# Kernel optimization log

Measured on AMD Instinct MI355X. Metric: run time of the kernel, lower is better.

The kernel has to match this reference:

```python
import jax, jax.numpy as jnp
import numpy as np

TAU = 2.0
BN_EPS = 1e-5
SG_ALPHA = 4.0
ATTN_SCALE = 0.125
NUM_HEADS = 8
T, B, C, H, W = 2, 16, 256, 64, 64


@jax.custom_vjp
def heaviside(x):
    return (x >= 0.0).astype(x.dtype)

def _hv_fwd(x):
    return (x >= 0.0).astype(x.dtype), x

def _hv_bwd(x, g):
    s = jax.nn.sigmoid(SG_ALPHA * x)
    return (g * SG_ALPHA * s * (1.0 - s),)

heaviside.defvjp(_hv_fwd, _hv_bwd)


def lif(x_seq, v_th):
    # MultiStepLIFNode: v <- v + (x - v)/tau ; spike = H(v - v_th); hard reset to 0 (detached)
    def step(v, x):
        v = v + (x - v) / TAU
        s = heaviside(v - v_th)
        v = v * (1.0 - jax.lax.stop_gradient(s))
        return v, s
    _, spikes = jax.lax.scan(step, jnp.zeros_like(x_seq[0]), x_seq)
    return spikes


def bn1d(x, gamma, beta, mean, var):
    # eval-mode BatchNorm1d over channel axis 2 of [T,B,C,N]
    inv = (gamma / jnp.sqrt(var + BN_EPS)).reshape(1, 1, -1, 1)
    shift = (beta - mean * gamma / jnp.sqrt(var + BN_EPS)).reshape(1, 1, -1, 1)
    return x * inv + shift


def to_heads(t):
    # [T,B,C,N] -> [T,B,h,N,d]
    t_, b_, c_, n_ = t.shape
    d = c_ // NUM_HEADS
    return t.transpose(0, 1, 3, 2).reshape(t_, b_, n_, NUM_HEADS, d).transpose(0, 1, 3, 2, 4)


def setup_inputs() -> dict:
    key = jax.random.key(0)
    ks = jax.random.split(key, 24)
    w_scale = 0.06  # ~1/sqrt(C)
    inp = {
        'x': jax.random.normal(ks[0], (T, B, C, H, W), jnp.float32),
        'wq': jax.random.normal(ks[1], (C, C), jnp.float32) * w_scale,
        'wk': jax.random.normal(ks[2], (C, C), jnp.float32) * w_scale,
        'wv': jax.random.normal(ks[3], (C, C), jnp.float32) * w_scale,
        'wp': jax.random.normal(ks[4], (C, C), jnp.float32) * w_scale,
        'bp': jax.random.normal(ks[5], (C,), jnp.float32) * 0.1,
    }
    i = 6
    for p in ('q', 'k', 'v', 'p'):
        inp[p + '_gamma'] = jax.random.uniform(ks[i], (C,), jnp.float32, 0.5, 1.5); i += 1
        inp[p + '_beta'] = jax.random.normal(ks[i], (C,), jnp.float32) * 0.1; i += 1
        inp[p + '_mean'] = jax.random.normal(ks[i], (C,), jnp.float32) * 0.1; i += 1
        inp[p + '_var'] = jax.random.uniform(ks[i], (C,), jnp.float32, 0.5, 1.5); i += 1
    return inp


def reference(x, wq, wk, wv, wp, bp,
              q_gamma, q_beta, q_mean, q_var,
              k_gamma, k_beta, k_mean, k_var,
              v_gamma, v_beta, v_mean, v_var,
              p_gamma, p_beta, p_mean, p_var):
    t_, b_, c_, h_, w_ = x.shape
    n_ = h_ * w_
    xs = lif(x, 1.0).reshape(t_, b_, c_, n_)  # proj_lif then flatten(3)
    # 1x1 conv == channel matmul, then BN, then LIF (binary spikes)
    q_out = lif(bn1d(jnp.einsum('oc,tbcn->tbon', wq, xs), q_gamma, q_beta, q_mean, q_var), 1.0)
    k_out = lif(bn1d(jnp.einsum('oc,tbcn->tbon', wk, xs), k_gamma, k_beta, k_mean, k_var), 1.0)
    v_out = lif(bn1d(jnp.einsum('oc,tbcn->tbon', wv, xs), v_gamma, v_beta, v_mean, v_var), 1.0)
    q = to_heads(q_out)
    k = to_heads(k_out)
    v = to_heads(v_out)
    # linear attention: (k^T @ v) then q @ (k^T v)
    kv = jnp.einsum('tbhnd,tbhne->tbhde', k, v)  # [T,B,h,d,d]
    attn = jnp.einsum('tbhnd,tbhde->tbhne', q, kv) * ATTN_SCALE
    attn = attn.transpose(0, 1, 2, 4, 3).reshape(t_, b_, c_, n_)
    s = lif(attn, 0.5)  # attn_lif with v_threshold=0.5
    out = jnp.einsum('oc,tbcn->tbon', wp, s) + bp.reshape(1, 1, -1, 1)
    out = bn1d(out, p_gamma, p_beta, p_mean, p_var).reshape(t_, b_, c_, h_, w_)
    return (out, xs, q_out, k_out, v_out)
```

## Files before the change

kernel.cpp:

```cpp
#include <hip/hip_runtime.h>
#include <cstdint>
#include <cstddef>

typedef __attribute__((ext_vector_type(8))) short short8;
typedef __attribute__((ext_vector_type(4))) float floatx4;
typedef __attribute__((ext_vector_type(4))) unsigned int uintx4;
typedef __attribute__((ext_vector_type(4))) unsigned short ushort4x;

#define DEV static __device__ __forceinline__

constexpr int NT = 2, NB = 16, NC = 256, NN = 4096, NHD = 8;
constexpr size_t NE1 = (size_t)NT * NB * NC * NN;
constexpr size_t TSTRIDE = (size_t)NB * NC * NN;

DEV unsigned short f2bf(float x) {
  unsigned int u = __builtin_bit_cast(unsigned int, x);
  unsigned int lsb = (u >> 16) & 1u;
  u += 0x7FFFu + lsb;
  return (unsigned short)(u >> 16);
}
DEV float bfb2f(unsigned short h) {
  unsigned int u = ((unsigned int)h) << 16;
  return __builtin_bit_cast(float, u);
}
DEV unsigned short spike2bf(float s) {
  return (unsigned short)(__builtin_bit_cast(unsigned int, s) >> 16);
}
DEV unsigned int pk2(unsigned short a, unsigned short b) {
  return (unsigned int)a | ((unsigned int)b << 16);
}
typedef __attribute__((address_space(3))) unsigned int lds_u32;
typedef __attribute__((address_space(1))) const unsigned int glb_u32;
DEV void gld_lds16(const void* g, void* l) {
  __builtin_amdgcn_global_load_lds((glb_u32*)g, (lds_u32*)l, 16, 0, 0);
}

__global__ __launch_bounds__(256) void prep_kernel(
    const float* __restrict__ wq, const float* __restrict__ wk, const float* __restrict__ wv,
    const float* __restrict__ wp, const float* __restrict__ bp,
    const float* __restrict__ qg, const float* __restrict__ qb, const float* __restrict__ qm, const float* __restrict__ qva,
    const float* __restrict__ kg, const float* __restrict__ kb, const float* __restrict__ km, const float* __restrict__ kva,
    const float* __restrict__ vg, const float* __restrict__ vb, const float* __restrict__ vm, const float* __restrict__ vva,
    const float* __restrict__ pg, const float* __restrict__ pb, const float* __restrict__ pm, const float* __restrict__ pva,
    unsigned short* __restrict__ Wqkv, unsigned short* __restrict__ Wp,
    float* __restrict__ invqkv, float* __restrict__ shqkv,
    float* __restrict__ invp, float* __restrict__ shp)
{
  int idx = blockIdx.x * 256 + threadIdx.x;
  if (idx < 196608) {
    int o = idx >> 8, c = idx & 255;
    const float* src = (o < 256) ? wq : (o < 512) ? wk : wv;
    float w = src[(size_t)(o & 255) * 256 + c];
    unsigned short h0 = f2bf(w);  float f0 = bfb2f(h0);
    float r1 = w - f0;
    unsigned short h1 = f2bf(r1); float f1 = bfb2f(h1);
    float r2 = r1 - f1;
    unsigned short h2 = f2bf(r2);
    Wqkv[idx] = h0; Wqkv[196608 + idx] = h1; Wqkv[393216 + idx] = h2;
  } else if (idx < 262144) {
    int j = idx - 196608;
    float w = wp[j];
    unsigned short h0 = f2bf(w);  float f0 = bfb2f(h0);
    float r1 = w - f0;
    unsigned short h1 = f2bf(r1); float f1 = bfb2f(h1);
    float r2 = r1 - f1;
    unsigned short h2 = f2bf(r2);
    Wp[j] = h0; Wp[65536 + j] = h1; Wp[131072 + j] = h2;
  } else if (idx < 262912) {
    int i = idx - 262144;
    int p = i >> 8, c = i & 255;
    float g  = (p == 0) ? qg[c] : (p == 1) ? kg[c] : vg[c];
    float be = (p == 0) ? qb[c] : (p == 1) ? kb[c] : vb[c];
    float mn = (p == 0) ? qm[c] : (p == 1) ? km[c] : vm[c];
    float vr = (p == 0) ? qva[c] : (p == 1) ? kva[c] : vva[c];
    float sq = sqrtf(vr + 1e-5f);
    invqkv[i] = g / sq;
    shqkv[i]  = be - (mn * g) / sq;
  } else if (idx < 263168) {
    int c = idx - 262912;
    float sq = sqrtf(pva[c] + 1e-5f);
    float iv = pg[c] / sq;
    invp[c] = iv;
    shp[c]  = pb[c] - (pm[c] * pg[c]) / sq + bp[c] * iv;
  }
}

__global__ __launch_bounds__(256) void lifx_kernel(const float* __restrict__ x,
                                                   float* __restrict__ xs_out,
                                                   unsigned short* __restrict__ xs_t)
{
  __shared__ float tile[2][64][65];
  const int nt = blockIdx.x, ct = blockIdx.y, b = blockIdx.z;
  const int tid = threadIdx.x;
  const int ci = tid >> 2, cq = tid & 3;
  const int n0 = nt * 64, c0 = ct * 64;
  const size_t rowbase = ((size_t)(b * NC + c0 + ci)) * NN + n0 + cq * 16;
  const float* px0 = x + rowbase;
  const float* px1 = x + rowbase + TSTRIDE;
  float* po0 = xs_out + rowbase;
  float* po1 = xs_out + rowbase + TSTRIDE;
  #pragma unroll
  for (int jj = 0; jj < 4; jj++) {
    floatx4 x0 = *(const floatx4*)(px0 + jj * 4);
    floatx4 x1 = *(const floatx4*)(px1 + jj * 4);
    floatx4 s0v, s1v;
    #pragma unroll
    for (int e = 0; e < 4; e++) {
      float v1 = x0[e] * 0.5f;
      float s0 = (v1 >= 1.0f) ? 1.0f : 0.0f;
      float vr = v1 * (1.0f - s0);
      float v2 = vr + (x1[e] - vr) * 0.5f;
      float s1 = (v2 >= 1.0f) ? 1.0f : 0.0f;
      s0v[e] = s0; s1v[e] = s1;
      tile[0][ci][cq * 16 + jj * 4 + e] = s0;
      tile[1][ci][cq * 16 + jj * 4 + e] = s1;
    }
    *(floatx4*)(po0 + jj * 4) = s0v;
    *(floatx4*)(po1 + jj * 4) = s1v;
  }
  __syncthreads();
  const int ni = tid >> 2, cg = tid & 3;
  #pragma unroll
  for (int t = 0; t < 2; t++) {
    unsigned short* dst = xs_t + ((size_t)((t * NB + b) * NN) + n0 + ni) * NC + c0 + cg * 16;
    uintx4 w0, w1;
    #pragma unroll
    for (int p2 = 0; p2 < 4; p2++) {
      w0[p2] = pk2(spike2bf(tile[t][cg * 16 + p2 * 2    ][ni]),
                   spike2bf(tile[t][cg * 16 + p2 * 2 + 1][ni]));
      w1[p2] = pk2(spike2bf(tile[t][cg * 16 + p2 * 2 + 8][ni]),
                   spike2bf(tile[t][cg * 16 + p2 * 2 + 9][ni]));
    }
    *(uintx4*)dst = w0;
    *(uintx4*)(dst + 8) = w1;
  }
}

__global__ __launch_bounds__(256, 3) void qkv_gemm(
    const unsigned short* __restrict__ xs_t,
    const unsigned short* __restrict__ Wsp,
    const float* __restrict__ invv, const float* __restrict__ shv,
    float* __restrict__ dq, float* __restrict__ dk, float* __restrict__ dv)
{
  __shared__ __align__(16) unsigned char smem[33280];
  unsigned short* Al = (unsigned short*)smem;
  unsigned short* Bl = (unsigned short*)(smem + 24576);
  float* yl = (float*)smem;
  const int nt = blockIdx.x, mt = blockIdx.y, b = blockIdx.z;
  const int tid = threadIdx.x;
  const int lane = tid & 63, quad = lane >> 4, l16 = lane & 15;
  const int wave = tid >> 6;
  const int tw = wave >> 1, wm = (wave & 1) * 64;
  floatx4 acc[4][4] = {};

  for (int k0 = 0; k0 < 256; k0 += 32) {
    __syncthreads();
    #pragma unroll
    for (int j = 0; j < 6; j++) {
      int ci = j * 256 + tid;
      int s = ci >> 9, j2 = ci & 511, row = j2 >> 2, kk = j2 & 3;
      const unsigned short* g = Wsp + (size_t)s * 196608 + (size_t)(mt * 128 + row) * 256 + k0 + kk * 8;
      gld_lds16(g, Al + ci * 8);
    }
    #pragma unroll
    for (int j = 0; j < 2; j++) {
      int ci = j * 256 + tid;
      int t = ci >> 8, j2 = ci & 255, row = j2 >> 2, kk = j2 & 3;
      const unsigned short* g = xs_t + ((size_t)((t * NB + b) * NN) + nt * 64 + row) * NC + k0 + kk * 8;
      gld_lds16(g, Bl + ci * 8);
    }
    __syncthreads();

    short8 bfr[4];
    #pragma unroll
    for (int ni = 0; ni < 4; ni++)
      bfr[ni] = *(const short8*)(Bl + ((size_t)(tw * 64 + ni * 16 + l16)) * 32 + quad * 8);
    #pragma unroll
    for (int mi = 0; mi < 4; mi++) {
      const int arow = wm + mi * 16 + l16;
      short8 a0 = *(const short8*)(Al + ((size_t)(          arow)) * 32 + quad * 8);
      short8 a1 = *(const short8*)(Al + ((size_t)(128  +   arow)) * 32 + quad * 8);
      short8 a2 = *(const short8*)(Al + ((size_t)(256  +   arow)) * 32 + quad * 8);
      #pragma unroll
      for (int ni = 0; ni < 4; ni++) {
        acc[mi][ni] = __builtin_amdgcn_mfma_f32_16x16x32_bf16(a0, bfr[ni], acc[mi][ni], 0, 0, 0);
        acc[mi][ni] = __builtin_amdgcn_mfma_f32_16x16x32_bf16(a1, bfr[ni], acc[mi][ni], 0, 0, 0);
        acc[mi][ni] = __builtin_amdgcn_mfma_f32_16x16x32_bf16(a2, bfr[ni], acc[mi][ni], 0, 0, 0);
      }
    }
  }
  __syncthreads();
  if (tw == 0) {
    #pragma unroll
    for (int mi = 0; mi < 4; mi++)
      #pragma unroll
      for (int r = 0; r < 4; r++)
        #pragma unroll
        for (int ni = 0; ni < 4; ni++)
          yl[(size_t)(wm + mi * 16 + quad * 4 + r) * 65 + ni * 16 + l16] = acc[mi][ni][r];
  }
  __syncthreads();
  if (tw == 1) {
    #pragma unroll
    for (int mi = 0; mi < 4; mi++) {
      #pragma unroll
      for (int r = 0; r < 4; r++) {
        const int lrow = wm + mi * 16 + quad * 4 + r;
        const int orow = mt * 128 + lrow;
        const float iv = invv[orow], sh = shv[orow];
        const int widx = orow >> 8, c = orow & 255;
        float* dst = (widx == 0) ? dq : (widx == 1) ? dk : dv;
        #pragma unroll
        for (int ni = 0; ni < 4; ni++) {
          const int n = nt * 64 + ni * 16 + l16;
          float y0 = yl[(size_t)lrow * 65 + ni * 16 + l16] * iv + sh;
          float y1 = acc[mi][ni][r] * iv + sh;
          float v1 = y0 * 0.5f;
          float s0 = (v1 >= 1.0f) ? 1.0f : 0.0f;
          float vr = v1 * (1.0f - s0);
          float v2 = vr + (y1 - vr) * 0.5f;
          float s1 = (v2 >= 1.0f) ? 1.0f : 0.0f;
          dst[(size_t)(b * NC + c) * NN + n] = s0;
          dst[(size_t)((NB + b) * NC + c) * NN + n] = s1;
        }
      }
    }
  }
}

__global__ __launch_bounds__(256) void kv_kernel(const float* __restrict__ kspk,
                                                 const float* __restrict__ vspk,
                                                 float* __restrict__ kvp)
{
  __shared__ __align__(16) unsigned short Kl[32][264];
  __shared__ __align__(16) unsigned short Vl[32][264];
  const int h = blockIdx.x, z = blockIdx.y, ch = blockIdx.z;
  const int tid = threadIdx.x;
  const int wave = tid >> 6, lane = tid & 63, quad = lane >> 4, l16 = lane & 15;
  const int dh = wave & 1, eh = wave >> 1;
  const size_t base = (size_t)z * NC * NN + (size_t)h * 32 * NN + (size_t)ch * 1024;
  floatx4 acc = {0.f, 0.f, 0.f, 0.f};
  for (int n0 = 0; n0 < 1024; n0 += 256) {
    __syncthreads();
    for (int i = tid; i < 2048; i += 256) {
      int row = i >> 6, c4 = (i & 63) * 4;
      const size_t g = base + (size_t)row * NN + n0 + c4;
      floatx4 kk = *(const floatx4*)(kspk + g);
      floatx4 vv = *(const floatx4*)(vspk + g);
      ushort4x ks, vs;
      #pragma unroll
      for (int e = 0; e < 4; e++) { ks[e] = spike2bf(kk[e]); vs[e] = spike2bf(vv[e]); }
      *(ushort4x*)&Kl[row][c4] = ks;
      *(ushort4x*)&Vl[row][c4] = vs;
    }
    __syncthreads();
    #pragma unroll
    for (int i = 0; i < 8; i++) {
      short8 ka = *(const short8*)&Kl[dh * 16 + l16][i * 32 + quad * 8];
      short8 vb = *(const short8*)&Vl[eh * 16 + l16][i * 32 + quad * 8];
      acc = __builtin_amdgcn_mfma_f32_16x16x32_bf16(ka, vb, acc, 0, 0, 0);
    }
  }
  float* o = kvp + ((size_t)((ch * 32 + z) * NHD + h)) * 1024;
  #pragma unroll
  for (int r = 0; r < 4; r++)
    o[(dh * 16 + quad * 4 + r) * 32 + eh * 16 + l16] = acc[r];
}

__global__ __launch_bounds__(256) void attn_kernel(const float* __restrict__ qspk,
                                                   const float* __restrict__ kvp,
                                                   unsigned short* __restrict__ s_t)
{
  __shared__ float kvl[2][32][32];
  const int nb = blockIdx.x, h = blockIdx.y, b = blockIdx.z;
  const int tid = threadIdx.x;
  for (int i = tid; i < 2048; i += 256) {
    int t = i >> 10, j = i & 1023;
    size_t o = ((size_t)((t * NB + b) * NHD + h) << 10) + j;
    float v = kvp[o] + kvp[o + 262144] + kvp[o + 524288] + kvp[o + 786432];
    kvl[t][j >> 5][j & 31] = v;
  }
  __syncthreads();
  const int n = nb * 256 + tid;
  float X[2][32];
  #pragma unroll
  for (int t = 0; t < 2; t++) {
    #pragma unroll
    for (int e = 0; e < 32; e++) X[t][e] = 0.f;
    const float* qp = qspk + ((size_t)((t * NB + b) * NC + h * 32)) * NN + n;
    #pragma unroll 4
    for (int d = 0; d < 32; d++) {
      float qv = qp[(size_t)d * NN];
      #pragma unroll
      for (int e = 0; e < 32; e++) X[t][e] += qv * kvl[t][d][e];
    }
  }
  unsigned short o0[32], o1[32];
  #pragma unroll
  for (int e = 0; e < 32; e++) {
    float a0 = X[0][e] * 0.125f;
    float a1 = X[1][e] * 0.125f;
    float v1 = a0 * 0.5f;
    float s0 = (v1 >= 0.5f) ? 1.f : 0.f;
    float vr = v1 * (1.f - s0);
    float v2 = vr + (a1 - vr) * 0.5f;
    float s1 = (v2 >= 0.5f) ? 1.f : 0.f;
    o0[e] = s0 != 0.f ? (unsigned short)0x3F80 : (unsigned short)0;
    o1[e] = s1 != 0.f ? (unsigned short)0x3F80 : (unsigned short)0;
  }
  unsigned short* dst0 = s_t + ((size_t)(b * NN) + n) * NC + h * 32;
  unsigned short* dst1 = s_t + ((size_t)((NB + b) * NN) + n) * NC + h * 32;
  #pragma unroll
  for (int g = 0; g < 4; g++) {
    uintx4 w0, w1;
    #pragma unroll
    for (int p = 0; p < 4; p++) {
      w0[p] = pk2(o0[g * 8 + p * 2], o0[g * 8 + p * 2 + 1]);
      w1[p] = pk2(o1[g * 8 + p * 2], o1[g * 8 + p * 2 + 1]);
    }
    *(uintx4*)(dst0 + g * 8) = w0;
    *(uintx4*)(dst1 + g * 8) = w1;
  }
}

__global__ __launch_bounds__(256, 3) void p_gemm(
    const unsigned short* __restrict__ s_t,
    const unsigned short* __restrict__ Wsp,
    const float* __restrict__ invv, const float* __restrict__ shv,
    float* __restrict__ dout)
{
  __shared__ __align__(16) unsigned char smem[32768];
  unsigned short* Al = (unsigned short*)smem;
  unsigned short* Bl = (unsigned short*)(smem + 24576);
  const int nt = blockIdx.x, mt = blockIdx.y, z = blockIdx.z;
  const int tid = threadIdx.x;
  const int lane = tid & 63, quad = lane >> 4, l16 = lane & 15;
  const int wave = tid >> 6;
  const int wm = (wave & 1) * 64, wn = (wave >> 1) * 64;
  floatx4 acc[4][4] = {};

  for (int k0 = 0; k0 < 256; k0 += 32) {
    __syncthreads();
    #pragma unroll
    for (int j = 0; j < 6; j++) {
      int ci = j * 256 + tid;
      int s = ci >> 9, j2 = ci & 511, row = j2 >> 2, kk = j2 & 3;
      const unsigned short* g = Wsp + (size_t)s * 65536 + (size_t)(mt * 128 + row) * 256 + k0 + kk * 8;
      gld_lds16(g, Al + ci * 8);
    }
    #pragma unroll
    for (int j = 0; j < 2; j++) {
      int ci = j * 256 + tid;
      int row = ci >> 2, kk = ci & 3;
      const unsigned short* g = s_t + ((size_t)(z * NN) + nt * 128 + row) * NC + k0 + kk * 8;
      gld_lds16(g, Bl + ci * 8);
    }
    __syncthreads();

    short8 bfr[4];
    #pragma unroll
    for (int ni = 0; ni < 4; ni++)
      bfr[ni] = *(const short8*)(Bl + ((size_t)(wn + ni * 16 + l16)) * 32 + quad * 8);
    #pragma unroll
    for (int mi = 0; mi < 4; mi++) {
      const int arow = wm + mi * 16 + l16;
      short8 a0 = *(const short8*)(Al + ((size_t)(        arow)) * 32 + quad * 8);
      short8 a1 = *(const short8*)(Al + ((size_t)(128 +   arow)) * 32 + quad * 8);
      short8 a2 = *(const short8*)(Al + ((size_t)(256 +   arow)) * 32 + quad * 8);
      #pragma unroll
      for (int ni = 0; ni < 4; ni++) {
        acc[mi][ni] = __builtin_amdgcn_mfma_f32_16x16x32_bf16(a0, bfr[ni], acc[mi][ni], 0, 0, 0);
        acc[mi][ni] = __builtin_amdgcn_mfma_f32_16x16x32_bf16(a1, bfr[ni], acc[mi][ni], 0, 0, 0);
        acc[mi][ni] = __builtin_amdgcn_mfma_f32_16x16x32_bf16(a2, bfr[ni], acc[mi][ni], 0, 0, 0);
      }
    }
  }
  #pragma unroll
  for (int mi = 0; mi < 4; mi++) {
    #pragma unroll
    for (int r = 0; r < 4; r++) {
      const int orow = mt * 128 + wm + mi * 16 + quad * 4 + r;
      const float iv = invv[orow], sh = shv[orow];
      #pragma unroll
      for (int ni = 0; ni < 4; ni++) {
        const int n = nt * 128 + wn + ni * 16 + l16;
        dout[((size_t)(z * NC + orow)) * NN + n] = acc[mi][ni][r] * iv + sh;
      }
    }
  }
}

extern "C" void kernel_launch(void* const* d_in, const int* in_sizes, int n_in,
                              void* d_out, int out_size, void* d_ws, size_t ws_size,
                              hipStream_t stream) {
  (void)in_sizes; (void)n_in; (void)out_size; (void)ws_size;
  const float* x  = (const float*)d_in[0];
  const float* wq = (const float*)d_in[1];
  const float* wk = (const float*)d_in[2];
  const float* wv = (const float*)d_in[3];
  const float* wp = (const float*)d_in[4];
  const float* bp = (const float*)d_in[5];
  const float* qg = (const float*)d_in[6],  *qb = (const float*)d_in[7];
  const float* qm = (const float*)d_in[8],  *qva = (const float*)d_in[9];
  const float* kg = (const float*)d_in[10], *kb = (const float*)d_in[11];
  const float* km = (const float*)d_in[12], *kva = (const float*)d_in[13];
  const float* vg = (const float*)d_in[14], *vb = (const float*)d_in[15];
  const float* vm = (const float*)d_in[16], *vva = (const float*)d_in[17];
  const float* pg = (const float*)d_in[18], *pb = (const float*)d_in[19];
  const float* pm = (const float*)d_in[20], *pva = (const float*)d_in[21];

  float* out = (float*)d_out;
  float* xs  = out + NE1;
  float* dq  = out + 2 * NE1;
  float* dk  = out + 3 * NE1;
  float* dv  = out + 4 * NE1;

  char* ws = (char*)d_ws;
  unsigned short* xs_t = (unsigned short*)ws;
  unsigned short* s_t  = (unsigned short*)ws;
  unsigned short* Wqkv = (unsigned short*)(ws + 67108864);
  unsigned short* Wp   = (unsigned short*)(ws + 68288512);
  float* kvp           = (float*)(ws + 68681728);
  float* invqkv        = (float*)(ws + 72876032);
  float* shqkv         = invqkv + 768;
  float* invp          = shqkv + 768;
  float* shp           = invp + 256;

  prep_kernel<<<1028, 256, 0, stream>>>(wq, wk, wv, wp, bp,
                                        qg, qb, qm, qva, kg, kb, km, kva,
                                        vg, vb, vm, vva, pg, pb, pm, pva,
                                        Wqkv, Wp, invqkv, shqkv, invp, shp);
  lifx_kernel<<<dim3(64, 4, 16), 256, 0, stream>>>(x, xs, xs_t);
  qkv_gemm<<<dim3(64, 6, 16), 256, 0, stream>>>(xs_t, Wqkv, invqkv, shqkv, dq, dk, dv);
  kv_kernel<<<dim3(8, 32, 4), 256, 0, stream>>>(dk, dv, kvp);
  attn_kernel<<<dim3(16, 8, 16), 256, 0, stream>>>(dq, kvp, s_t);
  p_gemm<<<dim3(32, 2, 32), 256, 0, stream>>>(s_t, Wp, invp, shp, out);
}
```

Measured before the change: 1.128 ms.

## Compute q·kv in attention kernel with bf16 MFMA using split-precision kv

Replaces the per-thread scalar FMA loop over 32x32 kv in attn_kernel with MFMA 16x16x32 bf16 instructions. The q spike tile is staged in padded LDS, and kv is split into high and low bf16 parts so that two MFMAs approximate fp32 precision. The aim is to remove the heavy FMA and LDS-broadcast cost. In exchange it writes output spikes as scattered 2-byte stores instead of 16-byte vectors, and the two-term bf16 split can still flip spikes that sit right at the threshold.

```diff
diff --git a/kernel.cpp b/kernel.cpp
--- a/kernel.cpp
+++ b/kernel.cpp
@@ -271,9 +271,11 @@
                                                    const float* __restrict__ kvp,
                                                    unsigned short* __restrict__ s_t)
 {
-  __shared__ float kvl[2][32][32];
+  __shared__ float kvl[2][32][33];
+  __shared__ __align__(8) float ql[32][258];
   const int nb = blockIdx.x, h = blockIdx.y, b = blockIdx.z;
   const int tid = threadIdx.x;
+  const int wave = tid >> 6, lane = tid & 63, quad = lane >> 4, l16 = lane & 15;
   for (int i = tid; i < 2048; i += 256) {
     int t = i >> 10, j = i & 1023;
     size_t o = ((size_t)((t * NB + b) * NHD + h) << 10) + j;
@@ -281,45 +283,68 @@
     kvl[t][j >> 5][j & 31] = v;
   }
   __syncthreads();
-  const int n = nb * 256 + tid;
-  float X[2][32];
+  short8 bf[2][2][2];
   #pragma unroll
   for (int t = 0; t < 2; t++) {
     #pragma unroll
-    for (int e = 0; e < 32; e++) X[t][e] = 0.f;
-    const float* qp = qspk + ((size_t)((t * NB + b) * NC + h * 32)) * NN + n;
-    #pragma unroll 4
-    for (int d = 0; d < 32; d++) {
-      float qv = qp[(size_t)d * NN];
-      #pragma unroll
-      for (int e = 0; e < 32; e++) X[t][e] += qv * kvl[t][d][e];
-    }
-  }
-  unsigned short o0[32], o1[32];
-  #pragma unroll
-  for (int e = 0; e < 32; e++) {
-    float a0 = X[0][e] * 0.125f;
-    float a1 = X[1][e] * 0.125f;
-    float v1 = a0 * 0.5f;
-    float s0 = (v1 >= 0.5f) ? 1.f : 0.f;
-    float vr = v1 * (1.f - s0);
-    float v2 = vr + (a1 - vr) * 0.5f;
-    float s1 = (v2 >= 0.5f) ? 1.f : 0.f;
-    o0[e] = s0 != 0.f ? (unsigned short)0x3F80 : (unsigned short)0;
-    o1[e] = s1 != 0.f ? (unsigned short)0x3F80 : (unsigned short)0;
-  }
-  unsigned short* dst0 = s_t + ((size_t)(b * NN) + n) * NC + h * 32;
-  unsigned short* dst1 = s_t + ((size_t)((NB + b) * NN) + n) * NC + h * 32;
-  #pragma unroll
-  for (int g = 0; g < 4; g++) {
-    uintx4 w0, w1;
-    #pragma unroll
-    for (int p = 0; p < 4; p++) {
-      w0[p] = pk2(o0[g * 8 + p * 2], o0[g * 8 + p * 2 + 1]);
-      w1[p] = pk2(o1[g * 8 + p * 2], o1[g * 8 + p * 2 + 1]);
-    }
-    *(uintx4*)(dst0 + g * 8) = w0;
-    *(uintx4*)(dst1 + g * 8) = w1;
+    for (int eh = 0; eh < 2; eh++) {
+      short8 bh, bl;
+      #pragma unroll
+      for (int j = 0; j < 8; j++) {
+        float v = kvl[t][quad * 8 + j][eh * 16 + l16];
+        unsigned short h0 = f2bf(v);
+        float lo = v - bfb2f(h0);
+        bh[j] = (short)h0;
+        bl[j] = (short)f2bf(lo);
+      }
+      bf[t][0][eh] = bh; bf[t][1][eh] = bl;
+    }
+  }
+  floatx4 acc[2][4][2] = {};
+  #pragma unroll
+  for (int t = 0; t < 2; t++) {
+    __syncthreads();
+    const float* qp = qspk + ((size_t)((t * NB + b) * NC + h * 32)) * NN + nb * 256;
+    for (int i = tid; i < 4096; i += 256) {
+      int row = i >> 7, c2 = (i & 127) * 2;
+      *(float2*)&ql[row][c2] = *(const float2*)(qp + (size_t)row * NN + c2);
+    }
+    __syncthreads();
+    #pragma unroll
+    for (int nt = 0; nt < 4; nt++) {
+      const int nrow = wave * 64 + nt * 16 + l16;
+      short8 af;
+      #pragma unroll
+      for (int j = 0; j < 8; j++)
+        af[j] = (short)spike2bf(ql[quad * 8 + j][nrow]);
+      #pragma unroll
+      for (int eh = 0; eh < 2; eh++) {
+        acc[t][nt][eh] = __builtin_amdgcn_mfma_f32_16x16x32_bf16(af, bf[t][0][eh], acc[t][nt][eh], 0, 0, 0);
+        acc[t][nt][eh] = __builtin_amdgcn_mfma_f32_16x16x32_bf16(af, bf[t][1][eh], acc[t][nt][eh], 0, 0, 0);
+      }
+    }
+  }
+  const int n0 = nb * 256 + wave * 64;
+  #pragma unroll
+  for (int nt = 0; nt < 4; nt++) {
+    #pragma unroll
+    for (int r = 0; r < 4; r++) {
+      const int n = n0 + nt * 16 + quad * 4 + r;
+      unsigned short* d0 = s_t + ((size_t)(b * NN) + n) * NC + h * 32 + l16;
+      unsigned short* d1 = s_t + ((size_t)((NB + b) * NN) + n) * NC + h * 32 + l16;
+      #pragma unroll
+      for (int eh = 0; eh < 2; eh++) {
+        float a0 = acc[0][nt][eh][r] * 0.125f;
+        float a1 = acc[1][nt][eh][r] * 0.125f;
+        float v1 = a0 * 0.5f;
+        float s0 = (v1 >= 0.5f) ? 1.f : 0.f;
+        float vr = v1 * (1.f - s0);
+        float v2 = vr + (a1 - vr) * 0.5f;
+        float s1 = (v2 >= 0.5f) ? 1.f : 0.f;
+        d0[eh * 16] = s0 != 0.f ? (unsigned short)0x3F80 : (unsigned short)0;
+        d1[eh * 16] = s1 != 0.f ? (unsigned short)0x3F80 : (unsigned short)0;
+      }
+    }
   }
 }
 
```

Result: faster. 1.093 ms (-3.1%).
